# Optimization experiments

Hardware: AMD Instinct MI355X
Metric: run time of the kernel (lower is better)

Reference implementation:

```python
import jax, jax.numpy as jnp
import numpy as np

N = 100000      # n_nodes
D = 64          # d_model
E = 1_600_000   # n_edges
L = 3           # n_layers


def setup_inputs() -> dict:
    key = jax.random.key(0)
    ks = jax.random.split(key, 2 + 2 * L)
    x = jax.random.normal(ks[0], (N, D), dtype=jnp.float32)
    edge_index = jax.random.randint(ks[1], (2, E), 0, N, dtype=jnp.int32)
    inp = {"x": x, "edge_index": edge_index}
    scale = 1.0 / np.sqrt(D)
    for i in range(L):
        # GCNConv weight (glorot-ish init) and zero bias
        inp[f"W{i}"] = jax.random.uniform(ks[2 + 2 * i], (D, D), jnp.float32, -scale, scale)
        inp[f"b{i}"] = jnp.zeros((D,), jnp.float32)
    return inp


def gcn_conv(x, W, b, src, dst, num_nodes):
    # PyG GCNConv: h = x @ W, then D^{-1/2}(A+I)D^{-1/2} aggregation, then + b
    h = x @ W  # [N, D]
    ones = jnp.ones(dst.shape, dtype=h.dtype)
    deg = jax.ops.segment_sum(ones, dst, num_segments=num_nodes)  # [N]
    deg_inv_sqrt = jnp.where(deg > 0, jax.lax.rsqrt(jnp.maximum(deg, 1.0)), 0.0)
    norm = deg_inv_sqrt[src] * deg_inv_sqrt[dst]  # [E+N]
    msg = h[src] * norm[:, None]                  # gather + scale  [E+N, D]
    out = jax.ops.segment_sum(msg, dst, num_segments=num_nodes)  # scatter-add [N, D]
    return out + b


def reference(x, edge_index, W0, b0, W1, b1, W2, b2):
    num_nodes = x.shape[0]
    loop = jnp.arange(num_nodes, dtype=edge_index.dtype)
    src = jnp.concatenate([edge_index[0], loop])  # add self-loops
    dst = jnp.concatenate([edge_index[1], loop])
    h = x
    for W, b in ((W0, b0), (W1, b1), (W2, b2)):
        h = gcn_conv(h, W, b, src, dst, num_nodes)
        # F.dropout(training=self.training) is identity in eval mode
    return h
```

## Files before the change

### kernel.cpp

```cpp
#include <hip/hip_runtime.h>
#include <hip/hip_bf16.h>

#define D 64
#define RSHIFT 9
#define BNODES 512
#define MAXB 256
#define BCAP 10240
#define FH 72

typedef unsigned short ushort_t;
typedef unsigned int uint_t;
typedef short short8 __attribute__((ext_vector_type(8)));
typedef float floatx4 __attribute__((ext_vector_type(4)));

__device__ inline uint_t pk_bf16(float x, float y) {
    uint_t ux = __float_as_uint(x); ux = ux + 0x7fffu + ((ux >> 16) & 1u);
    uint_t uy = __float_as_uint(y); uy = uy + 0x7fffu + ((uy >> 16) & 1u);
    return (ux >> 16) | (uy & 0xffff0000u);
}
__device__ inline ushort_t rnd_bf16(float x) {
    uint_t u = __float_as_uint(x); u = u + 0x7fffu + ((u >> 16) & 1u);
    return (ushort_t)(u >> 16);
}

__global__ __launch_bounds__(256) void k_bucket(const int* __restrict__ src,
                                                const int* __restrict__ dst,
                                                int* __restrict__ bcur,
                                                int* __restrict__ ebuf,
                                                int E, int nb) {
    __shared__ int lcnt[MAXB];
    __shared__ int lbase[MAXB];
    int t = threadIdx.x;
    lcnt[t] = 0;
    __syncthreads();
    int base = blockIdx.x * 2048 + t * 8;
    int sv[8], dv[8], sl[8];
    if (base + 7 < E) {
        int4 a0 = *(const int4*)(src + base);
        int4 a1 = *(const int4*)(src + base + 4);
        int4 b0 = *(const int4*)(dst + base);
        int4 b1 = *(const int4*)(dst + base + 4);
        sv[0]=a0.x; sv[1]=a0.y; sv[2]=a0.z; sv[3]=a0.w;
        sv[4]=a1.x; sv[5]=a1.y; sv[6]=a1.z; sv[7]=a1.w;
        dv[0]=b0.x; dv[1]=b0.y; dv[2]=b0.z; dv[3]=b0.w;
        dv[4]=b1.x; dv[5]=b1.y; dv[6]=b1.z; dv[7]=b1.w;
    } else {
        #pragma unroll
        for (int j = 0; j < 8; ++j) {
            dv[j] = (base + j < E) ? dst[base + j] : -1;
            sv[j] = (base + j < E) ? src[base + j] : 0;
        }
    }
    #pragma unroll
    for (int j = 0; j < 8; ++j) {
        if (dv[j] >= 0) {
            int b = dv[j] >> RSHIFT;
            sl[j] = atomicAdd(&lcnt[b], 1);
        }
    }
    __syncthreads();
    if (t < nb) { int c = lcnt[t]; if (c) lbase[t] = atomicAdd(&bcur[t], c); }
    __syncthreads();
    #pragma unroll
    for (int j = 0; j < 8; ++j) {
        if (dv[j] >= 0) {
            int b = dv[j] >> RSHIFT;
            int slot = lbase[b] + sl[j];
            if (slot < BCAP)
                ebuf[(size_t)b * BCAP + slot] = (sv[j] << RSHIFT) | (dv[j] & (BNODES - 1));
        }
    }
}

__global__ __launch_bounds__(256) void k_csr(const int* __restrict__ ebuf,
                                             const int* __restrict__ bcur,
                                             int* __restrict__ rowptr,
                                             int* __restrict__ ssrc,
                                             float* __restrict__ dis,
                                             int N, int nb) {
    __shared__ int lcnt[BNODES];
    __shared__ int lcur[BNODES];
    __shared__ int sums[256];
    __shared__ int red[4];
    int b = blockIdx.x;
    int t = threadIdx.x;
    int n = bcur[b];
    int node0 = b << RSHIFT;
    int pv = (t < b) ? bcur[t] : 0;
    int lane = t & 63, w = t >> 6;
    #pragma unroll
    for (int off = 1; off < 64; off <<= 1) pv += __shfl_xor(pv, off, 64);
    if (lane == 0) red[w] = pv;
    #pragma unroll
    for (int i = t; i < BNODES; i += 256) lcnt[i] = 0;
    __syncthreads();
    int base = red[0] + red[1] + red[2] + red[3];
    const int* seg = ebuf + (size_t)b * BCAP;
    for (int i = t * 4; i < n; i += 1024) {
        if (i + 3 < n) {
            int4 e = *(const int4*)(seg + i);
            atomicAdd(&lcnt[e.x & (BNODES - 1)], 1);
            atomicAdd(&lcnt[e.y & (BNODES - 1)], 1);
            atomicAdd(&lcnt[e.z & (BNODES - 1)], 1);
            atomicAdd(&lcnt[e.w & (BNODES - 1)], 1);
        } else {
            for (int j = 0; j < 4 && i + j < n; ++j)
                atomicAdd(&lcnt[seg[i + j] & (BNODES - 1)], 1);
        }
    }
    __syncthreads();
    int idx = t * 2;
    int v0 = lcnt[idx], v1 = lcnt[idx + 1];
    int s = v0 + v1;
    sums[t] = s;
    __syncthreads();
    for (int off = 1; off < 256; off <<= 1) {
        int x = (t >= off) ? sums[t - off] : 0;
        __syncthreads();
        sums[t] += x;
        __syncthreads();
    }
    int run = sums[t] - s;
    int node = node0 + idx;
    lcur[idx] = base + run;
    if (node < N) { rowptr[node] = base + run; dis[node] = rsqrtf((float)(v0 + 1)); }
    run += v0;
    lcur[idx + 1] = base + run;
    if (node + 1 < N) { rowptr[node + 1] = base + run; dis[node + 1] = rsqrtf((float)(v1 + 1)); }
    if (b == nb - 1 && t == 0) rowptr[N] = base + n;
    __syncthreads();
    for (int i = t * 4; i < n; i += 1024) {
        if (i + 3 < n) {
            int4 e = *(const int4*)(seg + i);
            int p0 = atomicAdd(&lcur[e.x & (BNODES - 1)], 1); ssrc[p0] = e.x >> RSHIFT;
            int p1 = atomicAdd(&lcur[e.y & (BNODES - 1)], 1); ssrc[p1] = e.y >> RSHIFT;
            int p2 = atomicAdd(&lcur[e.z & (BNODES - 1)], 1); ssrc[p2] = e.z >> RSHIFT;
            int p3 = atomicAdd(&lcur[e.w & (BNODES - 1)], 1); ssrc[p3] = e.w >> RSHIFT;
        } else {
            for (int j = 0; j < 4 && i + j < n; ++j) {
                int e = seg[i + j];
                int p = atomicAdd(&lcur[e & (BNODES - 1)], 1); ssrc[p] = e >> RSHIFT;
            }
        }
    }
}

__device__ __forceinline__ void stage_wt(const float* __restrict__ W,
                                         ushort_t* __restrict__ wt, int t) {
    const float4* W4 = (const float4*)W;
    for (int i = t; i < 1024; i += 256) {
        float4 w4 = W4[i];
        int k = i >> 4, n0 = (i & 15) * 4;
        wt[(n0 + 0) * FH + k] = rnd_bf16(w4.x);
        wt[(n0 + 1) * FH + k] = rnd_bf16(w4.y);
        wt[(n0 + 2) * FH + k] = rnd_bf16(w4.z);
        wt[(n0 + 3) * FH + k] = rnd_bf16(w4.w);
    }
}

__global__ __launch_bounds__(256) void k_gemm0(const float* __restrict__ x,
                                               const float* __restrict__ W,
                                               const float* __restrict__ dis,
                                               ushort_t* __restrict__ G, int N) {
    __shared__ ushort_t wt[64 * FH];
    int t = threadIdx.x;
    stage_wt(W, wt, t);
    __syncthreads();
    int wv = t >> 6, lane = t & 63;
    int m = lane & 15, quad = lane >> 4;
    int row = blockIdx.x * 64 + wv * 16 + m;
    long rowc = (row < N) ? row : (N - 1);
    float4 f0 = *(const float4*)(x + rowc * D + quad * 8);
    float4 f1 = *(const float4*)(x + rowc * D + quad * 8 + 4);
    float4 f2 = *(const float4*)(x + rowc * D + 32 + quad * 8);
    float4 f3 = *(const float4*)(x + rowc * D + 32 + quad * 8 + 4);
    union { short8 s; uint_t u[4]; } a0, a1;
    a0.u[0] = pk_bf16(f0.x, f0.y); a0.u[1] = pk_bf16(f0.z, f0.w);
    a0.u[2] = pk_bf16(f1.x, f1.y); a0.u[3] = pk_bf16(f1.z, f1.w);
    a1.u[0] = pk_bf16(f2.x, f2.y); a1.u[1] = pk_bf16(f2.z, f2.w);
    a1.u[2] = pk_bf16(f3.x, f3.y); a1.u[3] = pk_bf16(f3.z, f3.w);
    floatx4 acc[4];
    #pragma unroll
    for (int j = 0; j < 4; ++j) {
        short8 b0 = *(short8*)&wt[(j * 16 + m) * FH + quad * 8];
        short8 b1 = *(short8*)&wt[(j * 16 + m) * FH + 32 + quad * 8];
        floatx4 z = {0.f, 0.f, 0.f, 0.f};
        acc[j] = __builtin_amdgcn_mfma_f32_16x16x32_bf16(a0.s, b0, z, 0, 0, 0);
        acc[j] = __builtin_amdgcn_mfma_f32_16x16x32_bf16(a1.s, b1, acc[j], 0, 0, 0);
    }
    int rbase = blockIdx.x * 64 + wv * 16 + quad * 4;
    #pragma unroll
    for (int r = 0; r < 4; ++r) {
        int rr = rbase + r;
        if (rr < N) {
            float sc = dis[rr];
            #pragma unroll
            for (int j = 0; j < 4; ++j)
                G[(size_t)rr * D + j * 16 + m] = rnd_bf16(acc[j][r] * sc);
        }
    }
}

__device__ __forceinline__ void gather_half(const ushort_t* __restrict__ G,
                                            const int* __restrict__ ssrc,
                                            int beg, int end, int sub4, int c8,
                                            int node, float a[8]) {
    #pragma unroll
    for (int j = 0; j < 8; ++j) a[j] = 0.f;
    #define ACCUM(u)                                                       \
        {                                                                  \
            a[0] += __uint_as_float(u.x << 16);                            \
            a[1] += __uint_as_float(u.x & 0xffff0000u);                    \
            a[2] += __uint_as_float(u.y << 16);                            \
            a[3] += __uint_as_float(u.y & 0xffff0000u);                    \
            a[4] += __uint_as_float(u.z << 16);                            \
            a[5] += __uint_as_float(u.z & 0xffff0000u);                    \
            a[6] += __uint_as_float(u.w << 16);                            \
            a[7] += __uint_as_float(u.w & 0xffff0000u);                    \
        }
    if (sub4 == 0) {
        uint4 u = *(const uint4*)(G + (size_t)node * D + c8);
        ACCUM(u);
    }
    int e = beg + sub4;
    for (; e + 12 < end; e += 16) {
        int s0 = ssrc[e];
        int s1 = ssrc[e + 4];
        int s2 = ssrc[e + 8];
        int s3 = ssrc[e + 12];
        uint4 u0 = *(const uint4*)(G + (size_t)s0 * D + c8);
        uint4 u1 = *(const uint4*)(G + (size_t)s1 * D + c8);
        uint4 u2 = *(const uint4*)(G + (size_t)s2 * D + c8);
        uint4 u3 = *(const uint4*)(G + (size_t)s3 * D + c8);
        ACCUM(u0); ACCUM(u1); ACCUM(u2); ACCUM(u3);
    }
    if (e + 8 < end) {
        int s0 = ssrc[e], s1 = ssrc[e + 4], s2 = ssrc[e + 8];
        uint4 u0 = *(const uint4*)(G + (size_t)s0 * D + c8);
        uint4 u1 = *(const uint4*)(G + (size_t)s1 * D + c8);
        uint4 u2 = *(const uint4*)(G + (size_t)s2 * D + c8);
        ACCUM(u0); ACCUM(u1); ACCUM(u2);
    } else if (e + 4 < end) {
        int s0 = ssrc[e], s1 = ssrc[e + 4];
        uint4 u0 = *(const uint4*)(G + (size_t)s0 * D + c8);
        uint4 u1 = *(const uint4*)(G + (size_t)s1 * D + c8);
        ACCUM(u0); ACCUM(u1);
    } else if (e < end) {
        int s0 = ssrc[e];
        uint4 u0 = *(const uint4*)(G + (size_t)s0 * D + c8);
        ACCUM(u0);
    }
    #undef ACCUM
    #pragma unroll
    for (int j = 0; j < 8; ++j) {
        a[j] += __shfl_xor(a[j], 8, 64);
        a[j] += __shfl_xor(a[j], 16, 64);
    }
}

__global__ __launch_bounds__(256) void k_fagg(const ushort_t* __restrict__ G,
                                              const float* __restrict__ dis,
                                              const int* __restrict__ rowptr,
                                              const int* __restrict__ ssrc,
                                              const float* __restrict__ bias,
                                              const float* __restrict__ W,
                                              ushort_t* __restrict__ Gout,
                                              int N) {
    __shared__ ushort_t hbuf[64 * FH];
    __shared__ ushort_t wt[64 * FH];
    int t = threadIdx.x;
    stage_wt(W, wt, t);
    int wv = t >> 6, lane = t & 63;
    int half = lane >> 5;
    int sub4 = (lane >> 3) & 3;
    int c8 = (lane & 7) * 8;
    int gbase = blockIdx.x * 64;
    float4 bv0 = *(const float4*)(bias + c8);
    float4 bv1 = *(const float4*)(bias + c8 + 4);
    for (int ii = 0; ii < 8; ++ii) {
        int node = gbase + wv * 16 + ii * 2 + half;
        if (node < N) {
            int beg = rowptr[node], end = rowptr[node + 1];
            float di = dis[node];
            float a[8];
            gather_half(G, ssrc, beg, end, sub4, c8, node, a);
            if (sub4 == 0) {
                uint4 p;
                p.x = pk_bf16(a[0] * di + bv0.x, a[1] * di + bv0.y);
                p.y = pk_bf16(a[2] * di + bv0.z, a[3] * di + bv0.w);
                p.z = pk_bf16(a[4] * di + bv1.x, a[5] * di + bv1.y);
                p.w = pk_bf16(a[6] * di + bv1.z, a[7] * di + bv1.w);
                *(uint4*)&hbuf[(wv * 16 + ii * 2 + half) * FH + c8] = p;
            }
        }
    }
    __syncthreads();
    int m = lane & 15, quad = lane >> 4;
    short8 a0 = *(short8*)&hbuf[(wv * 16 + m) * FH + quad * 8];
    short8 a1 = *(short8*)&hbuf[(wv * 16 + m) * FH + 32 + quad * 8];
    floatx4 acc[4];
    #pragma unroll
    for (int j = 0; j < 4; ++j) {
        short8 b0 = *(short8*)&wt[(j * 16 + m) * FH + quad * 8];
        short8 b1 = *(short8*)&wt[(j * 16 + m) * FH + 32 + quad * 8];
        floatx4 z = {0.f, 0.f, 0.f, 0.f};
        acc[j] = __builtin_amdgcn_mfma_f32_16x16x32_bf16(a0, b0, z, 0, 0, 0);
        acc[j] = __builtin_amdgcn_mfma_f32_16x16x32_bf16(a1, b1, acc[j], 0, 0, 0);
    }
    int rbase = gbase + wv * 16 + quad * 4;
    #pragma unroll
    for (int r = 0; r < 4; ++r) {
        int row = rbase + r;
        if (row < N) {
            float sc = dis[row];
            #pragma unroll
            for (int j = 0; j < 4; ++j)
                Gout[(size_t)row * D + j * 16 + m] = rnd_bf16(acc[j][r] * sc);
        }
    }
}

__global__ __launch_bounds__(256) void k_agg(const ushort_t* __restrict__ G,
                                             const float* __restrict__ dis,
                                             const int* __restrict__ rowptr,
                                             const int* __restrict__ ssrc,
                                             const float* __restrict__ bias,
                                             float* __restrict__ out, int N) {
    int t = threadIdx.x;
    int wv = t >> 6, lane = t & 63;
    int half = lane >> 5;
    int sub4 = (lane >> 3) & 3;
    int c8 = (lane & 7) * 8;
    int node = blockIdx.x * 8 + wv * 2 + half;
    if (node >= N) return;
    int beg = rowptr[node], end = rowptr[node + 1];
    float di = dis[node];
    float a[8];
    gather_half(G, ssrc, beg, end, sub4, c8, node, a);
    if (sub4 == 0) {
        float4 bv0 = *(const float4*)(bias + c8);
        float4 bv1 = *(const float4*)(bias + c8 + 4);
        float4 r0, r1;
        r0.x = a[0] * di + bv0.x; r0.y = a[1] * di + bv0.y;
        r0.z = a[2] * di + bv0.z; r0.w = a[3] * di + bv0.w;
        r1.x = a[4] * di + bv1.x; r1.y = a[5] * di + bv1.y;
        r1.z = a[6] * di + bv1.z; r1.w = a[7] * di + bv1.w;
        float4* op = (float4*)(out + (size_t)node * D + c8);
        op[0] = r0;
        op[1] = r1;
    }
}


extern "C" void kernel_launch(void* const* d_in, const int* in_sizes, int n_in,
                              void* d_out, int out_size, void* d_ws, size_t ws_size,
                              hipStream_t stream) {
    const float* x  = (const float*)d_in[0];
    const int*   ei = (const int*)d_in[1];
    const float* W0 = (const float*)d_in[2];
    const float* b0 = (const float*)d_in[3];
    const float* W1 = (const float*)d_in[4];
    const float* b1 = (const float*)d_in[5];
    const float* W2 = (const float*)d_in[6];
    const float* b2 = (const float*)d_in[7];
    float* out = (float*)d_out;

    const int N = in_sizes[0] / D;
    const int E = in_sizes[1] / 2;
    const int* e_src = ei;
    const int* e_dst = ei + E;

    ushort_t* B0   = (ushort_t*)d_ws;
    ushort_t* B1   = B0 + (size_t)N * D;
    float* dis     = (float*)(B1 + (size_t)N * D);
    int*   rowptr  = (int*)(dis + N);
    int*   ssrc    = rowptr + (N + 1);
    int*   bcur    = ssrc + E;
    int*   ebuf    = (int*)d_ws;

    const int nb = (N + BNODES - 1) >> RSHIFT;
    const int gG64 = (N + 63) / 64;
    const int gAgg = (N + 7) / 8;

    hipMemsetAsync(bcur, 0, MAXB * sizeof(int), stream);
    k_bucket<<<(E + 2047) / 2048, 256, 0, stream>>>(e_src, e_dst, bcur, ebuf, E, nb);
    k_csr<<<nb, 256, 0, stream>>>(ebuf, bcur, rowptr, ssrc, dis, N, nb);

    k_gemm0<<<gG64, 256, 0, stream>>>(x, W0, dis, B0, N);
    k_fagg<<<gG64, 256, 0, stream>>>(B0, dis, rowptr, ssrc, b0, W1, B1, N);
    k_fagg<<<gG64, 256, 0, stream>>>(B1, dis, rowptr, ssrc, b1, W2, B0, N);
    k_agg<<<gAgg, 256, 0, stream>>>(B0, dis, rowptr, ssrc, b2, out, N);
}
```

Baseline: 297.4 us.

## Assign one 8-lane group per node in aggregation instead of splitting edges

The gather-aggregate now gives each node to a single 8-lane group that walks all of its edges. Before, the edges were split across four sub-groups and combined with cross-lane shuffles. This removes the shuffle reductions and the idle lanes in the epilogue, and a software-prefetched 8-wide index loop keeps more loads in flight. The cost is a longer serial edge loop per lane group, which adds imbalance for high-degree nodes and leaves fewer lanes working on each node's edges.

```diff
diff --git a/kernel.cpp b/kernel.cpp
--- a/kernel.cpp
+++ b/kernel.cpp
@@ -201,12 +201,19 @@
     }
 }
 
-__device__ __forceinline__ void gather_half(const ushort_t* __restrict__ G,
+__device__ __forceinline__ void gather_node(const ushort_t* __restrict__ G,
                                             const int* __restrict__ ssrc,
-                                            int beg, int end, int sub4, int c8,
+                                            int beg, int end, int c8,
                                             int node, float a[8]) {
-    #pragma unroll
-    for (int j = 0; j < 8; ++j) a[j] = 0.f;
+    uint4 su = *(const uint4*)(G + (size_t)node * D + c8);
+    a[0] = __uint_as_float(su.x << 16);
+    a[1] = __uint_as_float(su.x & 0xffff0000u);
+    a[2] = __uint_as_float(su.y << 16);
+    a[3] = __uint_as_float(su.y & 0xffff0000u);
+    a[4] = __uint_as_float(su.z << 16);
+    a[5] = __uint_as_float(su.z & 0xffff0000u);
+    a[6] = __uint_as_float(su.w << 16);
+    a[7] = __uint_as_float(su.w & 0xffff0000u);
     #define ACCUM(u)                                                       \
         {                                                                  \
             a[0] += __uint_as_float(u.x << 16);                            \
@@ -218,44 +225,53 @@
             a[6] += __uint_as_float(u.w << 16);                            \
             a[7] += __uint_as_float(u.w & 0xffff0000u);                    \
         }
-    if (sub4 == 0) {
-        uint4 u = *(const uint4*)(G + (size_t)node * D + c8);
-        ACCUM(u);
-    }
-    int e = beg + sub4;
-    for (; e + 12 < end; e += 16) {
-        int s0 = ssrc[e];
-        int s1 = ssrc[e + 4];
-        int s2 = ssrc[e + 8];
-        int s3 = ssrc[e + 12];
+    int e = beg;
+    int n8 = (end - beg) >> 3;
+    if (n8 > 0) {
+        int s0 = ssrc[e], s1 = ssrc[e + 1], s2 = ssrc[e + 2], s3 = ssrc[e + 3];
+        int s4 = ssrc[e + 4], s5 = ssrc[e + 5], s6 = ssrc[e + 6], s7 = ssrc[e + 7];
+        for (int ch = 0; ch < n8; ++ch) {
+            int ne = e + 8;
+            int t0 = s0, t1 = s1, t2 = s2, t3 = s3, t4 = s4, t5 = s5, t6 = s6, t7 = s7;
+            if (ch + 1 < n8) {
+                s0 = ssrc[ne];     s1 = ssrc[ne + 1]; s2 = ssrc[ne + 2]; s3 = ssrc[ne + 3];
+                s4 = ssrc[ne + 4]; s5 = ssrc[ne + 5]; s6 = ssrc[ne + 6]; s7 = ssrc[ne + 7];
+            }
+            uint4 u0 = *(const uint4*)(G + (size_t)t0 * D + c8);
+            uint4 u1 = *(const uint4*)(G + (size_t)t1 * D + c8);
+            uint4 u2 = *(const uint4*)(G + (size_t)t2 * D + c8);
+            uint4 u3 = *(const uint4*)(G + (size_t)t3 * D + c8);
+            uint4 u4 = *(const uint4*)(G + (size_t)t4 * D + c8);
+            uint4 u5 = *(const uint4*)(G + (size_t)t5 * D + c8);
+            uint4 u6 = *(const uint4*)(G + (size_t)t6 * D + c8);
+            uint4 u7 = *(const uint4*)(G + (size_t)t7 * D + c8);
+            ACCUM(u0); ACCUM(u1); ACCUM(u2); ACCUM(u3);
+            ACCUM(u4); ACCUM(u5); ACCUM(u6); ACCUM(u7);
+            e = ne;
+        }
+    }
+    if (e + 4 <= end) {
+        int s0 = ssrc[e], s1 = ssrc[e + 1], s2 = ssrc[e + 2], s3 = ssrc[e + 3];
         uint4 u0 = *(const uint4*)(G + (size_t)s0 * D + c8);
         uint4 u1 = *(const uint4*)(G + (size_t)s1 * D + c8);
         uint4 u2 = *(const uint4*)(G + (size_t)s2 * D + c8);
         uint4 u3 = *(const uint4*)(G + (size_t)s3 * D + c8);
         ACCUM(u0); ACCUM(u1); ACCUM(u2); ACCUM(u3);
-    }
-    if (e + 8 < end) {
-        int s0 = ssrc[e], s1 = ssrc[e + 4], s2 = ssrc[e + 8];
-        uint4 u0 = *(const uint4*)(G + (size_t)s0 * D + c8);
-        uint4 u1 = *(const uint4*)(G + (size_t)s1 * D + c8);
-        uint4 u2 = *(const uint4*)(G + (size_t)s2 * D + c8);
-        ACCUM(u0); ACCUM(u1); ACCUM(u2);
-    } else if (e + 4 < end) {
-        int s0 = ssrc[e], s1 = ssrc[e + 4];
+        e += 4;
+    }
+    if (e + 2 <= end) {
+        int s0 = ssrc[e], s1 = ssrc[e + 1];
         uint4 u0 = *(const uint4*)(G + (size_t)s0 * D + c8);
         uint4 u1 = *(const uint4*)(G + (size_t)s1 * D + c8);
         ACCUM(u0); ACCUM(u1);
-    } else if (e < end) {
+        e += 2;
+    }
+    if (e < end) {
         int s0 = ssrc[e];
         uint4 u0 = *(const uint4*)(G + (size_t)s0 * D + c8);
         ACCUM(u0);
     }
     #undef ACCUM
-    #pragma unroll
-    for (int j = 0; j < 8; ++j) {
-        a[j] += __shfl_xor(a[j], 8, 64);
-        a[j] += __shfl_xor(a[j], 16, 64);
-    }
 }
 
 __global__ __launch_bounds__(256) void k_fagg(const ushort_t* __restrict__ G,
@@ -271,27 +287,25 @@
     int t = threadIdx.x;
     stage_wt(W, wt, t);
     int wv = t >> 6, lane = t & 63;
-    int half = lane >> 5;
-    int sub4 = (lane >> 3) & 3;
+    int g = lane >> 3;
     int c8 = (lane & 7) * 8;
     int gbase = blockIdx.x * 64;
     float4 bv0 = *(const float4*)(bias + c8);
     float4 bv1 = *(const float4*)(bias + c8 + 4);
-    for (int ii = 0; ii < 8; ++ii) {
-        int node = gbase + wv * 16 + ii * 2 + half;
+    for (int ii = 0; ii < 2; ++ii) {
+        int idx = wv * 16 + ii * 8 + g;
+        int node = gbase + idx;
         if (node < N) {
             int beg = rowptr[node], end = rowptr[node + 1];
             float di = dis[node];
             float a[8];
-            gather_half(G, ssrc, beg, end, sub4, c8, node, a);
-            if (sub4 == 0) {
-                uint4 p;
-                p.x = pk_bf16(a[0] * di + bv0.x, a[1] * di + bv0.y);
-                p.y = pk_bf16(a[2] * di + bv0.z, a[3] * di + bv0.w);
-                p.z = pk_bf16(a[4] * di + bv1.x, a[5] * di + bv1.y);
-                p.w = pk_bf16(a[6] * di + bv1.z, a[7] * di + bv1.w);
-                *(uint4*)&hbuf[(wv * 16 + ii * 2 + half) * FH + c8] = p;
-            }
+            gather_node(G, ssrc, beg, end, c8, node, a);
+            uint4 p;
+            p.x = pk_bf16(a[0] * di + bv0.x, a[1] * di + bv0.y);
+            p.y = pk_bf16(a[2] * di + bv0.z, a[3] * di + bv0.w);
+            p.z = pk_bf16(a[4] * di + bv1.x, a[5] * di + bv1.y);
+            p.w = pk_bf16(a[6] * di + bv1.z, a[7] * di + bv1.w);
+            *(uint4*)&hbuf[idx * FH + c8] = p;
         }
     }
     __syncthreads();
@@ -328,27 +342,24 @@
                                              float* __restrict__ out, int N) {
     int t = threadIdx.x;
     int wv = t >> 6, lane = t & 63;
-    int half = lane >> 5;
-    int sub4 = (lane >> 3) & 3;
+    int g = lane >> 3;
     int c8 = (lane & 7) * 8;
-    int node = blockIdx.x * 8 + wv * 2 + half;
+    int node = blockIdx.x * 32 + wv * 8 + g;
     if (node >= N) return;
     int beg = rowptr[node], end = rowptr[node + 1];
     float di = dis[node];
     float a[8];
-    gather_half(G, ssrc, beg, end, sub4, c8, node, a);
-    if (sub4 == 0) {
-        float4 bv0 = *(const float4*)(bias + c8);
-        float4 bv1 = *(const float4*)(bias + c8 + 4);
-        float4 r0, r1;
-        r0.x = a[0] * di + bv0.x; r0.y = a[1] * di + bv0.y;
-        r0.z = a[2] * di + bv0.z; r0.w = a[3] * di + bv0.w;
-        r1.x = a[4] * di + bv1.x; r1.y = a[5] * di + bv1.y;
-        r1.z = a[6] * di + bv1.z; r1.w = a[7] * di + bv1.w;
-        float4* op = (float4*)(out + (size_t)node * D + c8);
-        op[0] = r0;
-        op[1] = r1;
-    }
+    gather_node(G, ssrc, beg, end, c8, node, a);
+    float4 bv0 = *(const float4*)(bias + c8);
+    float4 bv1 = *(const float4*)(bias + c8 + 4);
+    float4 r0, r1;
+    r0.x = a[0] * di + bv0.x; r0.y = a[1] * di + bv0.y;
+    r0.z = a[2] * di + bv0.z; r0.w = a[3] * di + bv0.w;
+    r1.x = a[4] * di + bv1.x; r1.y = a[5] * di + bv1.y;
+    r1.z = a[6] * di + bv1.z; r1.w = a[7] * di + bv1.w;
+    float4* op = (float4*)(out + (size_t)node * D + c8);
+    op[0] = r0;
+    op[1] = r1;
 }
 
 
@@ -380,7 +391,7 @@
 
     const int nb = (N + BNODES - 1) >> RSHIFT;
     const int gG64 = (N + 63) / 64;
-    const int gAgg = (N + 7) / 8;
+    const int gAgg = (N + 31) / 32;
 
     hipMemsetAsync(bcur, 0, MAXB * sizeof(int), stream);
     k_bucket<<<(E + 2047) / 2048, 256, 0, stream>>>(e_src, e_dst, bcur, ebuf, E, nb);
```

Measured after the change: 254.6 us. 1.17x faster.
